# Kernel optimization log

Measured on AMD Instinct MI355X. Metric: run time of the kernel, lower is better.

The kernel has to match this reference:

```python
import jax, jax.numpy as jnp
import numpy as np

THRESH = 1.0      # membrane_threshold
DECAY = 0.95      # membrane_decay
REFRAC = 2.0      # refractory_period
LR = 0.001        # learning_rate
MAX_RATE = 100.0  # max_spike_rate
DT = 1.0          # time_step (ms)


def _lif(v, r, I):
    """Event-driven LIF update, vectorized over (batch, neuron).
    Neurons are only updated where input current > 0 (as in the original
    gated per-element loop); elsewhere state is frozen.
    """
    active = I > 0
    refrac = r > 0
    v_int = v * DECAY + I
    fired = active & (~refrac) & (v_int >= THRESH)
    v_new = jnp.where(~active, v, jnp.where(refrac | fired, 0.0, v_int))
    r_new = jnp.where(~active, r,
                      jnp.where(refrac, r - 1.0,
                                jnp.where(fired, REFRAC, r)))
    return v_new, r_new, fired.astype(I.dtype)


def setup_inputs() -> dict:
    key = jax.random.key(0)
    k1, k2, k3, k4 = jax.random.split(key, 4)
    B, In, H, Out, T = 128, 1024, 4096, 1024, 100
    x = jax.random.uniform(k1, (B, In), dtype=jnp.float32)
    W1 = jax.random.normal(k2, (H, In), dtype=jnp.float32) / np.float32(np.sqrt(In))
    W2 = jax.random.normal(k3, (Out, H), dtype=jnp.float32) / np.float32(np.sqrt(H))
    noise = jax.random.uniform(k4, (T, B, In), dtype=jnp.float32)
    return {"x": x, "W1": W1, "W2": W2, "noise": noise, "time_steps": T}


def reference(x, W1, W2, noise, time_steps):
    B, In = x.shape
    H = W1.shape[0]
    Out = W2.shape[0]
    # rate coding: Bernoulli spikes per time step  -> (T, B, In)
    probs = jnp.clip(x * MAX_RATE, 0.0, MAX_RATE) * (DT / 1000.0)
    spikes_in = (noise < probs[None]).astype(x.dtype)

    def step(carry, inp):
        v_i, r_i, v_h, r_h, v_o, r_o, W1c, tp, tn, acc = carry
        t, s_in = inp
        # input layer LIF (current = encoded spikes)
        v_i, r_i, in_spk = _lif(v_i, r_i, s_in)
        # hidden layer: current = input spikes @ W1^T
        hid_I = in_spk @ W1c.T                      # (B, H)
        v_h, r_h, hid_spk = _lif(v_h, r_h, hid_I)
        # output layer: current = hidden spikes @ W2^T
        out_I = hid_spk @ W2.T                      # (B, Out)
        v_o, r_o, out_spk = _lif(v_o, r_o, out_I)
        acc = acc + out_spk
        # STDP every 10 steps
        stdp = (t % 10) == 0
        pre_m = in_spk.mean(0)                      # (In,)
        post_m = hid_spk.mean(0)                    # (H,)
        tp_n = 0.9 * tp + pre_m
        tn_n = 0.9 * tn + post_m
        tp = jnp.where(stdp, tp_n, tp)
        tn = jnp.where(stdp, tn_n, tn)
        both = (in_spk.sum() > 0) & (hid_spk.sum() > 0)
        dW = LR * (jnp.outer(tp_n, post_m).T - jnp.outer(pre_m, tn_n).T)  # (H, In)
        W1_new = jnp.clip(W1c + dW, -1.0, 1.0)
        W1c = jnp.where(stdp & both, W1_new, W1c)
        return (v_i, r_i, v_h, r_h, v_o, r_o, W1c, tp, tn, acc), None

    z = lambda *s: jnp.zeros(s, x.dtype)
    carry0 = (z(B, In), z(B, In), z(B, H), z(B, H), z(B, Out), z(B, Out),
              W1, z(In), z(H), z(B, Out))
    xs = (jnp.arange(time_steps), spikes_in)
    carry, _ = jax.lax.scan(step, carry0, xs)
    out_counts = carry[-1]
    return out_counts / time_steps
```

## Files before the change

kernel.cpp:

```cpp
#include <hip/hip_runtime.h>
#include <cstdint>
#include <cstddef>

#define BB   128
#define IN   1024
#define HID  4096
#define OUTN 1024
#define TSTEPS 100
#define KC   384

__global__ __launch_bounds__(256) void ttrans_k(const float* __restrict__ src,
                                                float* __restrict__ dst,
                                                int R, int C) {
  __shared__ float tile[32][33];
  int tx = threadIdx.x & 31;
  int ty = threadIdx.x >> 5;
  int c0 = blockIdx.x * 32, r0 = blockIdx.y * 32;
  #pragma unroll
  for (int j = 0; j < 32; j += 8)
    tile[ty + j][tx] = src[(size_t)(r0 + ty + j) * C + (c0 + tx)];
  __syncthreads();
  #pragma unroll
  for (int j = 0; j < 32; j += 8)
    dst[(size_t)(c0 + ty + j) * R + (r0 + tx)] = tile[tx][ty + j];
}

__device__ __forceinline__ unsigned char lif_f32(float I, float& v, float& r) {
  bool active = I > 0.0f;
  bool refrac = r > 0.0f;
  float vi = __fadd_rn(__fmul_rn(v, 0.95f), I);
  bool fired = active && !refrac && (vi >= 1.0f);
  float vn = !active ? v : ((refrac || fired) ? 0.0f : vi);
  float rn = !active ? r : (refrac ? (r - 1.0f) : (fired ? 2.0f : r));
  v = vn; r = rn;
  return fired ? (unsigned char)1 : (unsigned char)0;
}

#define GATHER8(SH)                                                              \
  {                                                                              \
    int k = ks;                                                                  \
    for (; k + 8 <= ke; k += 8) {                                                \
      unsigned o0 = ((unsigned)s_idx[k]     << SH) + cb;                         \
      unsigned o1 = ((unsigned)s_idx[k + 1] << SH) + cb;                         \
      unsigned o2 = ((unsigned)s_idx[k + 2] << SH) + cb;                         \
      unsigned o3 = ((unsigned)s_idx[k + 3] << SH) + cb;                         \
      unsigned o4 = ((unsigned)s_idx[k + 4] << SH) + cb;                         \
      unsigned o5 = ((unsigned)s_idx[k + 5] << SH) + cb;                         \
      unsigned o6 = ((unsigned)s_idx[k + 6] << SH) + cb;                         \
      unsigned o7 = ((unsigned)s_idx[k + 7] << SH) + cb;                         \
      float4 w0 = *reinterpret_cast<const float4*>(Wb + o0);                     \
      float4 w1 = *reinterpret_cast<const float4*>(Wb + o1);                     \
      float4 w2 = *reinterpret_cast<const float4*>(Wb + o2);                     \
      float4 w3 = *reinterpret_cast<const float4*>(Wb + o3);                     \
      float4 w4 = *reinterpret_cast<const float4*>(Wb + o4);                     \
      float4 w5 = *reinterpret_cast<const float4*>(Wb + o5);                     \
      float4 w6 = *reinterpret_cast<const float4*>(Wb + o6);                     \
      float4 w7 = *reinterpret_cast<const float4*>(Wb + o7);                     \
      a0 = __fadd_rn(a0, w0.x); a1 = __fadd_rn(a1, w0.y);                        \
      a2 = __fadd_rn(a2, w0.z); a3 = __fadd_rn(a3, w0.w);                        \
      a0 = __fadd_rn(a0, w1.x); a1 = __fadd_rn(a1, w1.y);                        \
      a2 = __fadd_rn(a2, w1.z); a3 = __fadd_rn(a3, w1.w);                        \
      a0 = __fadd_rn(a0, w2.x); a1 = __fadd_rn(a1, w2.y);                        \
      a2 = __fadd_rn(a2, w2.z); a3 = __fadd_rn(a3, w2.w);                        \
      a0 = __fadd_rn(a0, w3.x); a1 = __fadd_rn(a1, w3.y);                        \
      a2 = __fadd_rn(a2, w3.z); a3 = __fadd_rn(a3, w3.w);                        \
      a0 = __fadd_rn(a0, w4.x); a1 = __fadd_rn(a1, w4.y);                        \
      a2 = __fadd_rn(a2, w4.z); a3 = __fadd_rn(a3, w4.w);                        \
      a0 = __fadd_rn(a0, w5.x); a1 = __fadd_rn(a1, w5.y);                        \
      a2 = __fadd_rn(a2, w5.z); a3 = __fadd_rn(a3, w5.w);                        \
      a0 = __fadd_rn(a0, w6.x); a1 = __fadd_rn(a1, w6.y);                        \
      a2 = __fadd_rn(a2, w6.z); a3 = __fadd_rn(a3, w6.w);                        \
      a0 = __fadd_rn(a0, w7.x); a1 = __fadd_rn(a1, w7.y);                        \
      a2 = __fadd_rn(a2, w7.z); a3 = __fadd_rn(a3, w7.w);                        \
    }                                                                            \
    if (k + 4 <= ke) {                                                           \
      unsigned o0 = ((unsigned)s_idx[k]     << SH) + cb;                         \
      unsigned o1 = ((unsigned)s_idx[k + 1] << SH) + cb;                         \
      unsigned o2 = ((unsigned)s_idx[k + 2] << SH) + cb;                         \
      unsigned o3 = ((unsigned)s_idx[k + 3] << SH) + cb;                         \
      float4 w0 = *reinterpret_cast<const float4*>(Wb + o0);                     \
      float4 w1 = *reinterpret_cast<const float4*>(Wb + o1);                     \
      float4 w2 = *reinterpret_cast<const float4*>(Wb + o2);                     \
      float4 w3 = *reinterpret_cast<const float4*>(Wb + o3);                     \
      a0 = __fadd_rn(a0, w0.x); a1 = __fadd_rn(a1, w0.y);                        \
      a2 = __fadd_rn(a2, w0.z); a3 = __fadd_rn(a3, w0.w);                        \
      a0 = __fadd_rn(a0, w1.x); a1 = __fadd_rn(a1, w1.y);                        \
      a2 = __fadd_rn(a2, w1.z); a3 = __fadd_rn(a3, w1.w);                        \
      a0 = __fadd_rn(a0, w2.x); a1 = __fadd_rn(a1, w2.y);                        \
      a2 = __fadd_rn(a2, w2.z); a3 = __fadd_rn(a3, w2.w);                        \
      a0 = __fadd_rn(a0, w3.x); a1 = __fadd_rn(a1, w3.y);                        \
      a2 = __fadd_rn(a2, w3.z); a3 = __fadd_rn(a3, w3.w);                        \
      k += 4;                                                                    \
    }                                                                            \
    for (; k < ke; k++) {                                                        \
      unsigned oo = ((unsigned)s_idx[k] << SH) + cb;                             \
      float4 w = *reinterpret_cast<const float4*>(Wb + oo);                      \
      a0 = __fadd_rn(a0, w.x); a1 = __fadd_rn(a1, w.y);                          \
      a2 = __fadd_rn(a2, w.z); a3 = __fadd_rn(a3, w.w);                          \
    }                                                                            \
  }

__device__ __forceinline__ void hidden_body(
    int bx, int b, int tid,
    const float* __restrict__ noise_t, const float* __restrict__ x,
    const float* __restrict__ rin_in, float* __restrict__ rin_out,
    unsigned char* __restrict__ in_spk,
    const float* __restrict__ W1T,
    float* __restrict__ v_h, float* __restrict__ r_h,
    unsigned char* __restrict__ hid_spk,
    unsigned short* s_idx, int* s_off, int* wsum) {
  size_t ebase = (size_t)b * IN + (size_t)tid * 4;
  const float4 xv = *reinterpret_cast<const float4*>(x + ebase);
  const float4 nv = *reinterpret_cast<const float4*>(noise_t + ebase);
  const float4 rv = *reinterpret_cast<const float4*>(rin_in + ebase);
  float px[4] = {xv.x, xv.y, xv.z, xv.w};
  float pn[4] = {nv.x, nv.y, nv.z, nv.w};
  float pr[4] = {rv.x, rv.y, rv.z, rv.w};
  int f[4]; float rn[4];
  #pragma unroll
  for (int j = 0; j < 4; j++) {
    float p = __fmul_rn(px[j], 100.0f);
    p = fminf(fmaxf(p, 0.0f), 100.0f);
    p = __fmul_rn(p, 0.001f);
    bool s = pn[j] < p;
    bool refrac = pr[j] > 0.0f;
    bool fired = s && !refrac;
    rn[j] = !s ? pr[j] : (refrac ? (pr[j] - 1.0f) : 2.0f);
    f[j] = fired ? 1 : 0;
  }
  if (bx == 0) {
    *reinterpret_cast<float4*>(rin_out + ebase) = make_float4(rn[0], rn[1], rn[2], rn[3]);
    uchar4 sp; sp.x = (unsigned char)f[0]; sp.y = (unsigned char)f[1];
    sp.z = (unsigned char)f[2]; sp.w = (unsigned char)f[3];
    *reinterpret_cast<uchar4*>(in_spk + ebase) = sp;
  }
  int cnt = f[0] + f[1] + f[2] + f[3];

  int lane = tid & 63, wv = tid >> 6;
  int inc = cnt;
  #pragma unroll
  for (int d = 1; d < 64; d <<= 1) {
    int nn = __shfl_up(inc, d, 64);
    if (lane >= d) inc += nn;
  }
  if (lane == 63) wsum[wv] = inc;
  __syncthreads();
  int wbase = 0;
  #pragma unroll
  for (int w = 0; w < 4; w++) if (w < wv) wbase += wsum[w];
  int excl = wbase + inc - cnt;

  int o = excl, kb = tid * 4;
  if (f[0]) s_idx[o++] = (unsigned short)(kb);
  if (f[1]) s_idx[o++] = (unsigned short)(kb + 1);
  if (f[2]) s_idx[o++] = (unsigned short)(kb + 2);
  if (f[3]) s_idx[o++] = (unsigned short)(kb + 3);
  if (tid == 0)   s_off[0] = 0;
  if (tid == 96)  s_off[1] = excl;
  if (tid == 192) s_off[2] = excl;
  if (tid == 255) s_off[3] = excl + cnt;
  __syncthreads();

  int h0 = bx * 1024 + tid * 4;
  const char* Wb = (const char*)W1T;
  unsigned cb = (unsigned)h0 << 2;
  float t0 = 0.0f, t1 = 0.0f, t2 = 0.0f, t3 = 0.0f;
  #pragma unroll
  for (int p = 0; p < 3; p++) {
    int ks = s_off[p], ke = s_off[p + 1];
    float a0 = 0.0f, a1 = 0.0f, a2 = 0.0f, a3 = 0.0f;
    GATHER8(14)
    t0 = __fadd_rn(t0, a0); t1 = __fadd_rn(t1, a1);
    t2 = __fadd_rn(t2, a2); t3 = __fadd_rn(t3, a3);
  }
  size_t idx = (size_t)b * HID + h0;
  float4 vv = *reinterpret_cast<float4*>(v_h + idx);
  float4 rr = *reinterpret_cast<float4*>(r_h + idx);
  uchar4 sp;
  sp.x = lif_f32(t0, vv.x, rr.x);
  sp.y = lif_f32(t1, vv.y, rr.y);
  sp.z = lif_f32(t2, vv.z, rr.z);
  sp.w = lif_f32(t3, vv.w, rr.w);
  *reinterpret_cast<float4*>(v_h + idx) = vv;
  *reinterpret_cast<float4*>(r_h + idx) = rr;
  *reinterpret_cast<uchar4*>(hid_spk + idx) = sp;
}

__device__ __forceinline__ void out_body(
    int bx, int b, int tid,
    const unsigned char* __restrict__ hid_spk,
    const float* __restrict__ W2T,
    float* __restrict__ v_o, float* __restrict__ r_o,
    float* __restrict__ out_acc,
    unsigned short* s_idx, int* s_off, int* wsum, float* parts) {
  int lane = tid & 63, kg = tid >> 6;

  uint4 u = *reinterpret_cast<const uint4*>(hid_spk + (size_t)b * HID + tid * 16);
  unsigned ww[4] = {u.x, u.y, u.z, u.w};
  int cnt = 0;
  #pragma unroll
  for (int j = 0; j < 16; j++) cnt += (ww[j >> 2] >> ((j & 3) * 8)) & 0xff;

  int inc = cnt;
  #pragma unroll
  for (int d = 1; d < 64; d <<= 1) {
    int nn = __shfl_up(inc, d, 64);
    if (lane >= d) inc += nn;
  }
  if (lane == 63) wsum[kg] = inc;
  __syncthreads();
  int wbase = 0;
  #pragma unroll
  for (int w = 0; w < 4; w++) if (w < kg) wbase += wsum[w];
  int excl = wbase + inc - cnt;

  int oo = excl, kb = tid * 16;
  #pragma unroll
  for (int j = 0; j < 16; j++) {
    if ((ww[j >> 2] >> ((j & 3) * 8)) & 0xff) s_idx[oo++] = (unsigned short)(kb + j);
  }
  if ((tid % 24) == 0 && tid <= 240) s_off[tid / 24] = excl;
  if (tid == 255) s_off[11] = excl + cnt;
  __syncthreads();

  const int pstart = (kg == 0) ? 0 : (kg == 1) ? 3 : (kg == 2) ? 6 : 9;
  const int pend   = (kg == 0) ? 3 : (kg == 1) ? 6 : (kg == 2) ? 9 : 11;
  int col0 = lane * 4;
  const char* Wb = (const char*)W2T;
  unsigned cb = ((unsigned)(bx * 256 + col0)) << 2;
  for (int p = pstart; p < pend; p++) {
    int ks = s_off[p], ke = s_off[p + 1];
    float a0 = 0.0f, a1 = 0.0f, a2 = 0.0f, a3 = 0.0f;
    GATHER8(12)
    *reinterpret_cast<float4*>(parts + p * 256 + col0) = make_float4(a0, a1, a2, a3);
  }
  __syncthreads();

  float total = 0.0f;
  #pragma unroll
  for (int p = 0; p < 11; p++) total = __fadd_rn(total, parts[p * 256 + tid]);
  int o = bx * 256 + tid;
  size_t idx = (size_t)b * OUTN + o;
  float v = v_o[idx], r = r_o[idx];
  unsigned char fired = lif_f32(total, v, r);
  v_o[idx] = v; r_o[idx] = r;
  if (fired) out_acc[idx] = __fadd_rn(out_acc[idx], 1.0f);
}

__global__ __launch_bounds__(256) void hidden_k(
    const float* __restrict__ noise_t, const float* __restrict__ x,
    const float* __restrict__ rin_in, float* __restrict__ rin_out,
    unsigned char* __restrict__ in_spk,
    const float* __restrict__ W1T,
    float* __restrict__ v_h, float* __restrict__ r_h,
    unsigned char* __restrict__ hid_spk) {
  __shared__ unsigned short s_idx[IN];
  __shared__ int s_off[4];
  __shared__ int wsum[4];
  hidden_body(blockIdx.x, blockIdx.y, threadIdx.x, noise_t, x, rin_in, rin_out,
              in_spk, W1T, v_h, r_h, hid_spk, s_idx, s_off, wsum);
}

__global__ __launch_bounds__(256) void out_k(
    const unsigned char* __restrict__ hid_spk, const float* __restrict__ W2T,
    float* __restrict__ v_o, float* __restrict__ r_o, float* __restrict__ out_acc) {
  __shared__ unsigned short s_idx[HID];
  __shared__ int s_off[12];
  __shared__ int wsum[4];
  __shared__ float parts[11 * 256];
  out_body(blockIdx.x, blockIdx.y, threadIdx.x, hid_spk, W2T, v_o, r_o, out_acc,
           s_idx, s_off, wsum, parts);
}

__global__ __launch_bounds__(256) void step_k(
    const float* __restrict__ noise_t, const float* __restrict__ x,
    const float* __restrict__ rin_in, float* __restrict__ rin_out,
    unsigned char* __restrict__ in_spk,
    const float* __restrict__ W1T,
    float* __restrict__ v_h, float* __restrict__ r_h,
    unsigned char* __restrict__ hid_spk_w,
    const unsigned char* __restrict__ hid_spk_r,
    const float* __restrict__ W2T,
    float* __restrict__ v_o, float* __restrict__ r_o, float* __restrict__ out_acc) {
  __shared__ __align__(16) unsigned char smem[19520];
  int b = blockIdx.y;
  if (blockIdx.x < 4) {
    unsigned short* s_idx = (unsigned short*)smem;
    int* s_off = (int*)(smem + 2048);
    int* wsum  = (int*)(smem + 2064);
    hidden_body(blockIdx.x, b, threadIdx.x, noise_t, x, rin_in, rin_out,
                in_spk, W1T, v_h, r_h, hid_spk_w, s_idx, s_off, wsum);
  } else {
    unsigned short* s_idx = (unsigned short*)smem;
    int* s_off = (int*)(smem + 8192);
    int* wsum  = (int*)(smem + 8240);
    float* parts = (float*)(smem + 8256);
    out_body(blockIdx.x - 4, b, threadIdx.x, hid_spk_r, W2T, v_o, r_o, out_acc,
             s_idx, s_off, wsum, parts);
  }
}

#define NWSTAT ((IN + HID) / 4)
__global__ __launch_bounds__(256) void stats1_k(
    const unsigned char* __restrict__ in_spk, const unsigned char* __restrict__ hid_spk,
    unsigned* __restrict__ pcnt, int* __restrict__ flags) {
  int w = blockIdx.x * 256 + threadIdx.x;
  int r0 = blockIdx.y * 8;
  int lane = threadIdx.x & 63;
  unsigned s = 0;
  if (w < IN / 4) {
    const unsigned* p = (const unsigned*)in_spk;
    #pragma unroll
    for (int b = 0; b < 8; b++) s += p[(size_t)(r0 + b) * (IN / 4) + w];
    atomicAdd(pcnt + w, s);
    unsigned long long any = __ballot(s > 0);
    if (any && lane == 0) atomicOr(flags + 0, 1);
  } else {
    const unsigned* p = (const unsigned*)hid_spk;
    int w2 = w - IN / 4;
    #pragma unroll
    for (int b = 0; b < 8; b++) s += p[(size_t)(r0 + b) * (HID / 4) + w2];
    atomicAdd(pcnt + w, s);
    unsigned long long any = __ballot(s > 0);
    if (any && lane == 0) atomicOr(flags + 1, 1);
  }
}

__global__ __launch_bounds__(256) void apply2_k(
    float* __restrict__ W1T,
    const unsigned* __restrict__ pcnt,
    const float* __restrict__ tp_in, float* __restrict__ tp_out,
    const float* __restrict__ tn_in, float* __restrict__ tn_out,
    const int* __restrict__ flags) {
  size_t idx = (size_t)blockIdx.x * 256 + threadIdx.x;
  int i = (int)(idx >> 12);
  int h = (int)(idx & 4095);
  int cnt_i = (int)((pcnt[i >> 2] >> ((i & 3) * 8)) & 0xff);
  int ch = IN + h;
  int cnt_h = (int)((pcnt[ch >> 2] >> ((ch & 3) * 8)) & 0xff);
  float pm_i = __fmul_rn((float)cnt_i, 0.0078125f);
  float pm_h = __fmul_rn((float)cnt_h, 0.0078125f);
  float tpn = __fadd_rn(__fmul_rn(0.9f, tp_in[i]), pm_i);
  float tnn = __fadd_rn(__fmul_rn(0.9f, tn_in[h]), pm_h);
  if (h == 0) tp_out[i] = tpn;
  if (i == 0) tn_out[h] = tnn;
  if (!(flags[0] && flags[1])) return;
  float a  = __fmul_rn(tpn, pm_h);
  float b2 = __fmul_rn(pm_i, tnn);
  float d  = __fmul_rn(0.001f, __fsub_rn(a, b2));
  float w  = __fadd_rn(W1T[idx], d);
  w = fminf(fmaxf(w, -1.0f), 1.0f);
  W1T[idx] = w;
}

__global__ __launch_bounds__(256) void scale_k(const float* __restrict__ acc,
                                               float* __restrict__ out) {
  int j = blockIdx.x * 256 + threadIdx.x;
  out[j] = __fdiv_rn(acc[j], 100.0f);
}

extern "C" void kernel_launch(void* const* d_in, const int* in_sizes, int n_in,
                              void* d_out, int out_size, void* d_ws, size_t ws_size,
                              hipStream_t stream) {
  (void)in_sizes; (void)n_in; (void)out_size; (void)ws_size;
  const float* x     = (const float*)d_in[0];
  const float* W1    = (const float*)d_in[1];
  const float* W2    = (const float*)d_in[2];
  const float* noise = (const float*)d_in[3];

  char* ws = (char*)d_ws;
  size_t off = 0;
  auto alloc = [&](size_t bytes) -> char* {
    char* p = ws + off;
    off += (bytes + 255) & ~(size_t)255;
    return p;
  };
  float* W1T   = (float*)alloc((size_t)IN * HID * 4);
  float* W2T   = (float*)alloc((size_t)HID * OUTN * 4);
  float* v_h   = (float*)alloc((size_t)BB * HID * 4);
  float* r_h   = (float*)alloc((size_t)BB * HID * 4);
  float* v_o   = (float*)alloc((size_t)BB * OUTN * 4);
  float* r_o   = (float*)alloc((size_t)BB * OUTN * 4);
  float* rinA  = (float*)alloc((size_t)BB * IN * 4);
  float* rinB  = (float*)alloc((size_t)BB * IN * 4);
  float* acc   = (float*)alloc((size_t)BB * OUTN * 4);
  float* tpA   = (float*)alloc((size_t)IN * 4);
  float* tpB   = (float*)alloc((size_t)IN * 4);
  float* tnA   = (float*)alloc((size_t)HID * 4);
  float* tnB   = (float*)alloc((size_t)HID * 4);
  unsigned char* in_spk   = (unsigned char*)alloc((size_t)BB * IN);
  unsigned char* hid_spkA = (unsigned char*)alloc((size_t)BB * HID);
  unsigned char* hid_spkB = (unsigned char*)alloc((size_t)BB * HID);
  unsigned* pcnt = (unsigned*)alloc((size_t)10 * NWSTAT * 4);
  int* flags   = (int*)alloc(2 * 10 * sizeof(int));

  hipMemsetAsync(v_h, 0, (size_t)BB * HID * 4, stream);
  hipMemsetAsync(r_h, 0, (size_t)BB * HID * 4, stream);
  hipMemsetAsync(v_o, 0, (size_t)BB * OUTN * 4, stream);
  hipMemsetAsync(r_o, 0, (size_t)BB * OUTN * 4, stream);
  hipMemsetAsync(rinA, 0, (size_t)BB * IN * 4, stream);
  hipMemsetAsync(acc, 0, (size_t)BB * OUTN * 4, stream);
  hipMemsetAsync(tpA, 0, (size_t)IN * 4, stream);
  hipMemsetAsync(tnA, 0, (size_t)HID * 4, stream);
  hipMemsetAsync(pcnt, 0, (size_t)10 * NWSTAT * 4, stream);
  hipMemsetAsync(flags, 0, 2 * 10 * sizeof(int), stream);

  ttrans_k<<<dim3(IN / 32, HID / 32), 256, 0, stream>>>(W1, W1T, HID, IN);
  ttrans_k<<<dim3(HID / 32, OUTN / 32), 256, 0, stream>>>(W2, W2T, OUTN, HID);

  float* rin_in = rinA;
  float* rin_out = rinB;
  float* tp_in = tpA; float* tp_out = tpB;
  float* tn_in = tnA; float* tn_out = tnB;

  hidden_k<<<dim3(HID / 1024, BB), 256, 0, stream>>>(noise, x, rin_in, rin_out, in_spk,
                                                     W1T, v_h, r_h, hid_spkA);
  {
    unsigned* pc = pcnt;  int* fl = flags;
    stats1_k<<<dim3(NWSTAT / 256, 16), 256, 0, stream>>>(in_spk, hid_spkA, pc, fl);
    apply2_k<<<(IN * HID) / 256, 256, 0, stream>>>(W1T, pc, tp_in, tp_out,
                                                   tn_in, tn_out, fl);
    float* t1 = tp_in; tp_in = tp_out; tp_out = t1;
    float* t2 = tn_in; tn_in = tn_out; tn_out = t2;
  }
  { float* tmpp = rin_in; rin_in = rin_out; rin_out = tmpp; }

  for (int t = 1; t < TSTEPS; t++) {
    const float* nz = noise + (size_t)t * BB * IN;
    unsigned char* hs_w = (t & 1) ? hid_spkB : hid_spkA;
    unsigned char* hs_r = (t & 1) ? hid_spkA : hid_spkB;
    step_k<<<dim3(8, BB), 256, 0, stream>>>(nz, x, rin_in, rin_out, in_spk,
                                            W1T, v_h, r_h, hs_w, hs_r,
                                            W2T, v_o, r_o, acc);
    if (t % 10 == 0) {
      unsigned* pc = pcnt + (size_t)NWSTAT * (t / 10);
      int* fl = flags + 2 * (t / 10);
      stats1_k<<<dim3(NWSTAT / 256, 16), 256, 0, stream>>>(in_spk, hs_w, pc, fl);
      apply2_k<<<(IN * HID) / 256, 256, 0, stream>>>(W1T, pc, tp_in, tp_out,
                                                     tn_in, tn_out, fl);
      float* t1 = tp_in; tp_in = tp_out; tp_out = t1;
      float* t2 = tn_in; tn_in = tn_out; tn_out = t2;
    }
    float* tmpp = rin_in; rin_in = rin_out; rin_out = tmpp;
  }

  unsigned char* hs_last = ((TSTEPS - 1) & 1) ? hid_spkB : hid_spkA;
  out_k<<<dim3(OUTN / 256, BB), 256, 0, stream>>>(hs_last, W2T, v_o, r_o, acc);

  scale_k<<<(BB * OUTN) / 256, 256, 0, stream>>>(acc, (float*)d_out);
}
```

Before: 1.487 ms.

## Double step kernel block size and split sparse gather across two thread groups

The fused per-timestep kernel now launches 512 threads per block instead of 256. In the hidden branch the spike-index list is split into partitions: the first 256 threads gather two of them and the second 256 gather the third, with the results combined through shared memory before the LIF update. The output branch spreads its 11 gather partitions over 8 waves instead of 4. This aims to hide gather latency with more in-flight loads per block. The cost is extra barriers and shared-memory reductions, and the summation order changes, which may move float results slightly.

```diff
diff --git a/kernel.cpp b/kernel.cpp
--- a/kernel.cpp
+++ b/kernel.cpp
@@ -100,6 +100,39 @@
     }                                                                            \
   }
 
+__device__ __forceinline__ int encode4(
+    int bx, int b, int tid,
+    const float* __restrict__ noise_t, const float* __restrict__ x,
+    const float* __restrict__ rin_in, float* __restrict__ rin_out,
+    unsigned char* __restrict__ in_spk, int f[4]) {
+  size_t ebase = (size_t)b * IN + (size_t)tid * 4;
+  const float4 xv = *reinterpret_cast<const float4*>(x + ebase);
+  const float4 nv = *reinterpret_cast<const float4*>(noise_t + ebase);
+  const float4 rv = *reinterpret_cast<const float4*>(rin_in + ebase);
+  float px[4] = {xv.x, xv.y, xv.z, xv.w};
+  float pn[4] = {nv.x, nv.y, nv.z, nv.w};
+  float pr[4] = {rv.x, rv.y, rv.z, rv.w};
+  float rn[4];
+  #pragma unroll
+  for (int j = 0; j < 4; j++) {
+    float p = __fmul_rn(px[j], 100.0f);
+    p = fminf(fmaxf(p, 0.0f), 100.0f);
+    p = __fmul_rn(p, 0.001f);
+    bool s = pn[j] < p;
+    bool refrac = pr[j] > 0.0f;
+    bool fired = s && !refrac;
+    rn[j] = !s ? pr[j] : (refrac ? (pr[j] - 1.0f) : 2.0f);
+    f[j] = fired ? 1 : 0;
+  }
+  if (bx == 0) {
+    *reinterpret_cast<float4*>(rin_out + ebase) = make_float4(rn[0], rn[1], rn[2], rn[3]);
+    uchar4 sp; sp.x = (unsigned char)f[0]; sp.y = (unsigned char)f[1];
+    sp.z = (unsigned char)f[2]; sp.w = (unsigned char)f[3];
+    *reinterpret_cast<uchar4*>(in_spk + ebase) = sp;
+  }
+  return f[0] + f[1] + f[2] + f[3];
+}
+
 __device__ __forceinline__ void hidden_body(
     int bx, int b, int tid,
     const float* __restrict__ noise_t, const float* __restrict__ x,
@@ -109,32 +142,8 @@
     float* __restrict__ v_h, float* __restrict__ r_h,
     unsigned char* __restrict__ hid_spk,
     unsigned short* s_idx, int* s_off, int* wsum) {
-  size_t ebase = (size_t)b * IN + (size_t)tid * 4;
-  const float4 xv = *reinterpret_cast<const float4*>(x + ebase);
-  const float4 nv = *reinterpret_cast<const float4*>(noise_t + ebase);
-  const float4 rv = *reinterpret_cast<const float4*>(rin_in + ebase);
-  float px[4] = {xv.x, xv.y, xv.z, xv.w};
-  float pn[4] = {nv.x, nv.y, nv.z, nv.w};
-  float pr[4] = {rv.x, rv.y, rv.z, rv.w};
-  int f[4]; float rn[4];
-  #pragma unroll
-  for (int j = 0; j < 4; j++) {
-    float p = __fmul_rn(px[j], 100.0f);
-    p = fminf(fmaxf(p, 0.0f), 100.0f);
-    p = __fmul_rn(p, 0.001f);
-    bool s = pn[j] < p;
-    bool refrac = pr[j] > 0.0f;
-    bool fired = s && !refrac;
-    rn[j] = !s ? pr[j] : (refrac ? (pr[j] - 1.0f) : 2.0f);
-    f[j] = fired ? 1 : 0;
-  }
-  if (bx == 0) {
-    *reinterpret_cast<float4*>(rin_out + ebase) = make_float4(rn[0], rn[1], rn[2], rn[3]);
-    uchar4 sp; sp.x = (unsigned char)f[0]; sp.y = (unsigned char)f[1];
-    sp.z = (unsigned char)f[2]; sp.w = (unsigned char)f[3];
-    *reinterpret_cast<uchar4*>(in_spk + ebase) = sp;
-  }
-  int cnt = f[0] + f[1] + f[2] + f[3];
+  int f[4];
+  int cnt = encode4(bx, b, tid, noise_t, x, rin_in, rin_out, in_spk, f);
 
   int lane = tid & 63, wv = tid >> 6;
   int inc = cnt;
@@ -272,7 +281,7 @@
            s_idx, s_off, wsum, parts);
 }
 
-__global__ __launch_bounds__(256) void step_k(
+__global__ __launch_bounds__(512) void step_k(
     const float* __restrict__ noise_t, const float* __restrict__ x,
     const float* __restrict__ rin_in, float* __restrict__ rin_out,
     unsigned char* __restrict__ in_spk,
@@ -283,20 +292,151 @@
     const float* __restrict__ W2T,
     float* __restrict__ v_o, float* __restrict__ r_o, float* __restrict__ out_acc) {
   __shared__ __align__(16) unsigned char smem[19520];
+  int tid = threadIdx.x;
   int b = blockIdx.y;
+  int lane = tid & 63, wv = tid >> 6;
+
   if (blockIdx.x < 4) {
     unsigned short* s_idx = (unsigned short*)smem;
     int* s_off = (int*)(smem + 2048);
     int* wsum  = (int*)(smem + 2064);
-    hidden_body(blockIdx.x, b, threadIdx.x, noise_t, x, rin_in, rin_out,
-                in_spk, W1T, v_h, r_h, hid_spk_w, s_idx, s_off, wsum);
+    float* sA  = (float*)(smem + 2080);
+    float* p2  = (float*)(smem + 6176);
+    int bx = blockIdx.x;
+    int f[4]; int cnt = 0, inc = 0;
+    if (tid < 256) {
+      cnt = encode4(bx, b, tid, noise_t, x, rin_in, rin_out, in_spk, f);
+      inc = cnt;
+      #pragma unroll
+      for (int d = 1; d < 64; d <<= 1) {
+        int nn = __shfl_up(inc, d, 64);
+        if (lane >= d) inc += nn;
+      }
+      if (lane == 63) wsum[wv] = inc;
+    }
+    __syncthreads();
+    if (tid < 256) {
+      int wbase = 0;
+      #pragma unroll
+      for (int w = 0; w < 4; w++) if (w < wv) wbase += wsum[w];
+      int excl = wbase + inc - cnt;
+      int o = excl, kb = tid * 4;
+      if (f[0]) s_idx[o++] = (unsigned short)(kb);
+      if (f[1]) s_idx[o++] = (unsigned short)(kb + 1);
+      if (f[2]) s_idx[o++] = (unsigned short)(kb + 2);
+      if (f[3]) s_idx[o++] = (unsigned short)(kb + 3);
+      if (tid == 0)   s_off[0] = 0;
+      if (tid == 96)  s_off[1] = excl;
+      if (tid == 192) s_off[2] = excl;
+      if (tid == 255) s_off[3] = excl + cnt;
+    }
+    __syncthreads();
+
+    int g  = tid >> 8;
+    int tl = tid & 255;
+    int h0 = bx * 1024 + tl * 4;
+    const char* Wb = (const char*)W1T;
+    unsigned cb = (unsigned)h0 << 2;
+    if (g == 0) {
+      float t0 = 0.0f, t1 = 0.0f, t2 = 0.0f, t3 = 0.0f;
+      #pragma unroll
+      for (int p = 0; p < 2; p++) {
+        int ks = s_off[p], ke = s_off[p + 1];
+        float a0 = 0.0f, a1 = 0.0f, a2 = 0.0f, a3 = 0.0f;
+        GATHER8(14)
+        t0 = __fadd_rn(t0, a0); t1 = __fadd_rn(t1, a1);
+        t2 = __fadd_rn(t2, a2); t3 = __fadd_rn(t3, a3);
+      }
+      *reinterpret_cast<float4*>(sA + tl * 4) = make_float4(t0, t1, t2, t3);
+    } else {
+      int ks = s_off[2], ke = s_off[3];
+      float a0 = 0.0f, a1 = 0.0f, a2 = 0.0f, a3 = 0.0f;
+      GATHER8(14)
+      *reinterpret_cast<float4*>(p2 + tl * 4) = make_float4(a0, a1, a2, a3);
+    }
+    __syncthreads();
+
+    if (tid < 256) {
+      float4 sa = *reinterpret_cast<const float4*>(sA + tid * 4);
+      float4 pb = *reinterpret_cast<const float4*>(p2 + tid * 4);
+      float t0 = __fadd_rn(sa.x, pb.x);
+      float t1 = __fadd_rn(sa.y, pb.y);
+      float t2 = __fadd_rn(sa.z, pb.z);
+      float t3 = __fadd_rn(sa.w, pb.w);
+      size_t idx = (size_t)b * HID + bx * 1024 + tid * 4;
+      float4 vv = *reinterpret_cast<float4*>(v_h + idx);
+      float4 rr = *reinterpret_cast<float4*>(r_h + idx);
+      uchar4 sp;
+      sp.x = lif_f32(t0, vv.x, rr.x);
+      sp.y = lif_f32(t1, vv.y, rr.y);
+      sp.z = lif_f32(t2, vv.z, rr.z);
+      sp.w = lif_f32(t3, vv.w, rr.w);
+      *reinterpret_cast<float4*>(v_h + idx) = vv;
+      *reinterpret_cast<float4*>(r_h + idx) = rr;
+      *reinterpret_cast<uchar4*>(hid_spk_w + idx) = sp;
+    }
   } else {
     unsigned short* s_idx = (unsigned short*)smem;
     int* s_off = (int*)(smem + 8192);
     int* wsum  = (int*)(smem + 8240);
     float* parts = (float*)(smem + 8256);
-    out_body(blockIdx.x - 4, b, threadIdx.x, hid_spk_r, W2T, v_o, r_o, out_acc,
-             s_idx, s_off, wsum, parts);
+    int bx = blockIdx.x - 4;
+    unsigned ww[4];
+    int cnt = 0, inc = 0;
+    if (tid < 256) {
+      uint4 u = *reinterpret_cast<const uint4*>(hid_spk_r + (size_t)b * HID + tid * 16);
+      ww[0] = u.x; ww[1] = u.y; ww[2] = u.z; ww[3] = u.w;
+      #pragma unroll
+      for (int j = 0; j < 16; j++) cnt += (ww[j >> 2] >> ((j & 3) * 8)) & 0xff;
+      inc = cnt;
+      #pragma unroll
+      for (int d = 1; d < 64; d <<= 1) {
+        int nn = __shfl_up(inc, d, 64);
+        if (lane >= d) inc += nn;
+      }
+      if (lane == 63) wsum[wv] = inc;
+    }
+    __syncthreads();
+    if (tid < 256) {
+      int wbase = 0;
+      #pragma unroll
+      for (int w = 0; w < 4; w++) if (w < wv) wbase += wsum[w];
+      int excl = wbase + inc - cnt;
+      int oo = excl, kb = tid * 16;
+      #pragma unroll
+      for (int j = 0; j < 16; j++) {
+        if ((ww[j >> 2] >> ((j & 3) * 8)) & 0xff) s_idx[oo++] = (unsigned short)(kb + j);
+      }
+      if ((tid % 24) == 0 && tid <= 240) s_off[tid / 24] = excl;
+      if (tid == 255) s_off[11] = excl + cnt;
+    }
+    __syncthreads();
+
+    const int pst[8] = {0, 2, 4, 5, 6, 7, 8, 10};
+    const int pen[8] = {2, 4, 5, 6, 7, 8, 10, 11};
+    int pstart = pst[wv], pend = pen[wv];
+    int col0 = lane * 4;
+    const char* Wb = (const char*)W2T;
+    unsigned cb = ((unsigned)(bx * 256 + col0)) << 2;
+    for (int p = pstart; p < pend; p++) {
+      int ks = s_off[p], ke = s_off[p + 1];
+      float a0 = 0.0f, a1 = 0.0f, a2 = 0.0f, a3 = 0.0f;
+      GATHER8(12)
+      *reinterpret_cast<float4*>(parts + p * 256 + col0) = make_float4(a0, a1, a2, a3);
+    }
+    __syncthreads();
+
+    if (tid < 256) {
+      float total = 0.0f;
+      #pragma unroll
+      for (int p = 0; p < 11; p++) total = __fadd_rn(total, parts[p * 256 + tid]);
+      int o = bx * 256 + tid;
+      size_t idx = (size_t)b * OUTN + o;
+      float v = v_o[idx], r = r_o[idx];
+      unsigned char fired = lif_f32(total, v, r);
+      v_o[idx] = v; r_o[idx] = r;
+      if (fired) out_acc[idx] = __fadd_rn(out_acc[idx], 1.0f);
+    }
   }
 }
 
@@ -413,8 +553,8 @@
   float* tp_in = tpA; float* tp_out = tpB;
   float* tn_in = tnA; float* tn_out = tnB;
 
-  hidden_k<<<dim3(HID / 1024, BB), 256, 0, stream>>>(noise, x, rin_in, rin_out, in_spk,
-                                                     W1T, v_h, r_h, hid_spkA);
+  hidden_k<<<dim3(4, BB), 256, 0, stream>>>(noise, x, rin_in, rin_out, in_spk,
+                                            W1T, v_h, r_h, hid_spkA);
   {
     unsigned* pc = pcnt;  int* fl = flags;
     stats1_k<<<dim3(NWSTAT / 256, 16), 256, 0, stream>>>(in_spk, hid_spkA, pc, fl);
@@ -429,7 +569,7 @@
     const float* nz = noise + (size_t)t * BB * IN;
     unsigned char* hs_w = (t & 1) ? hid_spkB : hid_spkA;
     unsigned char* hs_r = (t & 1) ? hid_spkA : hid_spkB;
-    step_k<<<dim3(8, BB), 256, 0, stream>>>(nz, x, rin_in, rin_out, in_spk,
+    step_k<<<dim3(8, BB), 512, 0, stream>>>(nz, x, rin_in, rin_out, in_spk,
                                             W1T, v_h, r_h, hs_w, hs_r,
                                             W2T, v_o, r_o, acc);
     if (t % 10 == 0) {
@@ -445,7 +585,7 @@
   }
 
   unsigned char* hs_last = ((TSTEPS - 1) & 1) ? hid_spkB : hid_spkA;
-  out_k<<<dim3(OUTN / 256, BB), 256, 0, stream>>>(hs_last, W2T, v_o, r_o, acc);
+  out_k<<<dim3(4, BB), 256, 0, stream>>>(hs_last, W2T, v_o, r_o, acc);
 
   scale_k<<<(BB * OUTN) / 256, 256, 0, stream>>>(acc, (float*)d_out);
 }
```

New measurement: 1.487 ms. About the same (-0.0%).
